# Kernel tuning notes

Measured on AMD Instinct MI355X. Metric: run time of the kernel, lower is better.

Reference implementation:

```python
import jax, jax.numpy as jnp
import numpy as np
from jax import lax


def _conv(x, w, b):
    y = lax.conv_general_dilated(x, w, window_strides=(1, 1), padding='SAME',
                                 dimension_numbers=('NCHW', 'OIHW', 'NCHW'))
    return y + b[None, :, None, None]


def _maxpool2(x):
    return lax.reduce_window(x, -jnp.inf, lax.max,
                             window_dimensions=(1, 1, 2, 2),
                             window_strides=(1, 1, 2, 2), padding='VALID')


def setup_inputs() -> dict:
    key = jax.random.key(0)
    ks = jax.random.split(key, 11)
    f32 = jnp.float32
    return {
        'x': jax.random.normal(ks[0], (512, 1, 112, 112), f32),
        'w_conv1': jax.random.normal(ks[1], (8, 1, 3, 3), f32) * 0.1,
        'b_conv1': jax.random.normal(ks[2], (8,), f32) * 0.1,
        'w_conv2': jax.random.normal(ks[3], (16, 8, 3, 3), f32) * 0.1,
        'b_conv2': jax.random.normal(ks[4], (16,), f32) * 0.1,
        'w_patch': jax.random.normal(ks[5], (4, 64), f32) * 0.1,
        'b_patch': jax.random.normal(ks[6], (4,), f32) * 0.1,
        'w_fc1': jax.random.normal(ks[7], (64, 784), f32) * 0.05,
        'b_fc1': jax.random.normal(ks[8], (64,), f32) * 0.05,
        'w_fc2': jax.random.normal(ks[9], (10, 64), f32) * 0.05,
        'b_fc2': jax.random.normal(ks[10], (10,), f32) * 0.05,
    }


def reference(x, w_conv1, b_conv1, w_conv2, b_conv2, w_patch, b_patch,
              w_fc1, b_fc1, w_fc2, b_fc2):
    B = x.shape[0]
    h = _maxpool2(jax.nn.relu(_conv(x, w_conv1, b_conv1)))        # [B,8,56,56]
    f = _maxpool2(jax.nn.relu(_conv(h, w_conv2, b_conv2)))        # [B,16,28,28]
    C, H, W = f.shape[1], f.shape[2], f.shape[3]
    # im2col: 2x2 non-overlapping spatial patches, flattened as (C,2,2) -> 64
    p = f.reshape(B, C, H // 2, 2, W // 2, 2)
    p = p.transpose(0, 2, 4, 1, 3, 5).reshape(B, (H // 2) * (W // 2), C * 4)  # [B,196,64]
    pf = jnp.einsum('bpk,ok->bpo', p, w_patch) + b_patch          # [B,196,4]
    pf = pf.reshape(B, -1)                                        # [B,784]
    h1 = jax.nn.relu(pf @ w_fc1.T + b_fc1)
    logits = h1 @ w_fc2.T + b_fc2
    return jax.nn.log_softmax(logits, axis=-1)
```

## Files before the change

### kernel.cpp

```cpp
#include <hip/hip_runtime.h>


#define HS 58
#define FSTR 33

typedef _Float16 half2_t __attribute__((ext_vector_type(2)));
typedef _Float16 f16x8 __attribute__((ext_vector_type(8)));
typedef float f32x4 __attribute__((ext_vector_type(4)));
typedef float f32x2 __attribute__((ext_vector_type(2)));

__device__ __forceinline__ unsigned pack_f16(float a, float b) {
  union { half2_t h; unsigned u; } z;
  z.h[0] = (_Float16)a;
  z.h[1] = (_Float16)b;
  return z.u;
}

__device__ __forceinline__ half2_t as_h2(unsigned u) {
  union { unsigned u; half2_t h; } z;
  z.u = u;
  return z.h;
}

__device__ __forceinline__ f16x8 as_f16x8(uint4 u) {
  union { uint4 u; f16x8 f; } z;
  z.u = u;
  return z.f;
}

__device__ __forceinline__ float fdot2_(half2_t a, half2_t b, float c) {
#if __has_builtin(__builtin_amdgcn_fdot2)
  return __builtin_amdgcn_fdot2(a, b, c, false);
#else
  return c + (float)a[0] * (float)b[0] + (float)a[1] * (float)b[1];
#endif
}

__global__ __launch_bounds__(1024, 8) void k_all(
    const float* __restrict__ x, const float* __restrict__ w1,
    const float* __restrict__ b1, const float* __restrict__ w2,
    const float* __restrict__ b2, const float* __restrict__ wp,
    const float* __restrict__ bp, const float* __restrict__ w_fc1,
    const float* __restrict__ b_fc1, const float* __restrict__ w_fc2,
    const float* __restrict__ b_fc2, float* __restrict__ out) {
  __shared__ __align__(16) unsigned hsu[HS * HS * 4];
  __shared__ __align__(16) unsigned bwl[768];
  __shared__ __align__(16) unsigned wps[128];
  __shared__ __align__(16) unsigned fsu[98 * FSTR];
  __shared__ __align__(16) float pfl[784];
  __shared__ float h1s[64];
  const int tid = threadIdx.x;
  const int b = blockIdx.x;
  const int l = tid & 63;
  const int wv = __builtin_amdgcn_readfirstlane(tid >> 6);
  const float* xb = x + (long)b * 12544;
  const float bpv = bp[tid & 3];

  if (tid < 228) {
    int i = tid, hr, hc;
    if (i < 58) { hr = 0; hc = i; }
    else if (i < 116) { hr = 57; hc = i - 58; }
    else if (i < 172) { hr = i - 115; hc = 0; }
    else { hr = i - 171; hc = 57; }
    *(uint4*)(hsu + (hr * HS + hc) * 4) = make_uint4(0u, 0u, 0u, 0u);
  }
  if (tid < 768) {
    int t = tid, oc = t / 48, rem = t - oc * 48;
    int tap = rem >> 2, w = rem & 3;
    unsigned v = 0u;
    if (tap < 9)
      v = pack_f16(w2[(oc * 8 + 2 * w) * 9 + tap],
                   w2[(oc * 8 + 2 * w + 1) * 9 + tap]);
    bwl[t] = v;
  }
  if (tid >= 768 && tid < 896) {
    int t = tid - 768;
    int i = t >> 2, ot = t & 3;
    int l0 = 2 * i, l1 = 2 * i + 1;
    wps[t] = pack_f16(wp[ot * 64 + (l0 & 15) * 4 + (l0 >> 4)],
                      wp[ot * 64 + (l1 & 15) * 4 + (l1 >> 4)]);
  }

  for (int task = tid; task < 3136; task += 1024) {
    int gr = task / 56, gc = task - gr * 56;
    float win[4][4];
    int iy0 = 2 * gr - 1, ix0 = 2 * gc - 1;
    if (gr >= 1 && gr <= 54 && gc >= 1 && gc <= 54) {
      const float* xp = xb + iy0 * 112 + ix0;
#pragma unroll
      for (int rr = 0; rr < 4; ++rr)
#pragma unroll
        for (int qq = 0; qq < 4; ++qq)
          win[rr][qq] = xp[rr * 112 + qq];
    } else {
#pragma unroll
      for (int rr = 0; rr < 4; ++rr) {
        int iy = iy0 + rr;
        bool yok = (unsigned)iy < 112u;
#pragma unroll
        for (int qq = 0; qq < 4; ++qq) {
          int ix = ix0 + qq;
          win[rr][qq] = (yok && (unsigned)ix < 112u) ? xb[iy * 112 + ix] : 0.f;
        }
      }
    }
    float hv[8];
#pragma unroll
    for (int ch = 0; ch < 8; ++ch) {
      f32x2 sA = {0.f, 0.f};
      f32x2 sB = {0.f, 0.f};
#pragma unroll
      for (int ty = 0; ty < 3; ++ty)
#pragma unroll
        for (int tx = 0; tx < 3; ++tx) {
          float wk = w1[ch * 9 + ty * 3 + tx];
          f32x2 wkk = {wk, wk};
          f32x2 xa = {win[ty][tx], win[ty][tx + 1]};
          f32x2 xb2 = {win[ty + 1][tx], win[ty + 1][tx + 1]};
          sA = __builtin_elementwise_fma(xa, wkk, sA);
          sB = __builtin_elementwise_fma(xb2, wkk, sB);
        }
      f32x2 sm = __builtin_elementwise_max(sA, sB);
      float m = fmaxf(sm.x, sm.y);
      hv[ch] = fmaxf(m + b1[ch], 0.f);
    }
    uint4 hw;
    hw.x = pack_f16(hv[0], hv[1]);
    hw.y = pack_f16(hv[2], hv[3]);
    hw.z = pack_f16(hv[4], hv[5]);
    hw.w = pack_f16(hv[6], hv[7]);
    *(uint4*)(hsu + ((gr + 1) * HS + gc + 1) * 4) = hw;
  }
  __syncthreads();

  {
    const int q = l >> 4;
    const int yoff = 2 * ((l >> 3) & 1) + ((l >> 1) & 1);
    const int xoff = 2 * ((l >> 2) & 1) + (l & 1);
    int poff[3];
#pragma unroll
    for (int kk = 0; kk < 3; ++kk) {
      int t = kk * 4 + q;
      int tt = t < 9 ? t : 8;
      int ty = tt / 3, tx = tt - ty * 3;
      poff[kk] = ((yoff + ty) * HS + xoff + tx) * 4;
    }
    uint4 bu0 = *(const uint4*)(bwl + ((l & 15) * 12 + 0 + q) * 4);
    uint4 bu1 = *(const uint4*)(bwl + ((l & 15) * 12 + 4 + q) * 4);
    uint4 bu2 = *(const uint4*)(bwl + ((l & 15) * 12 + 8 + q) * 4);
    const float b2v = b2[l & 15];
    _Float16* fsh = (_Float16*)fsu;

    for (int c = 0; c < 2; ++c) {
#pragma unroll 2
      for (int p_l = wv; p_l < 98; p_l += 16) {
        int p = c * 98 + p_l;
        int py = p / 14, px = p - py * 14;
        int pb = (4 * py * HS + 4 * px) * 4;
        uint4 a0u = *(const uint4*)(hsu + pb + poff[0]);
        uint4 a1u = *(const uint4*)(hsu + pb + poff[1]);
        uint4 a2u = *(const uint4*)(hsu + pb + poff[2]);
        f32x4 acc = {0.f, 0.f, 0.f, 0.f};
        acc = __builtin_amdgcn_mfma_f32_16x16x32_f16(as_f16x8(a0u), as_f16x8(bu0), acc, 0, 0, 0);
        acc = __builtin_amdgcn_mfma_f32_16x16x32_f16(as_f16x8(a1u), as_f16x8(bu1), acc, 0, 0, 0);
        acc = __builtin_amdgcn_mfma_f32_16x16x32_f16(as_f16x8(a2u), as_f16x8(bu2), acc, 0, 0, 0);
        float mx = fmaxf(fmaxf(acc[0], acc[1]), fmaxf(acc[2], acc[3]));
        float fv = fmaxf(mx + b2v, 0.f);
        fsh[p_l * (2 * FSTR) + l] = (_Float16)fv;
      }
      __syncthreads();
      if (tid < 392) {
        int row = tid >> 2, ot = tid & 3;
        const unsigned* fr = fsu + row * FSTR;
        float acc = 0.f;
#pragma unroll
        for (int i = 0; i < 32; ++i)
          acc = fdot2_(as_h2(fr[i]), as_h2(wps[i * 4 + ot]), acc);
        pfl[(c * 98 + row) * 4 + ot] = acc + bpv;
      }
      __syncthreads();
    }
  }

  {
    int j = tid >> 4, q16 = tid & 15;
    const float* wrow = w_fc1 + j * 784;
    float acc = 0.f;
    for (int lp = q16; lp < 196; lp += 16) {
      float4 w4 = *(const float4*)(wrow + lp * 4);
      float4 p4 = *(const float4*)(pfl + lp * 4);
      acc += w4.x * p4.x + w4.y * p4.y + w4.z * p4.z + w4.w * p4.w;
    }
    acc += __shfl_down(acc, 8, 16);
    acc += __shfl_down(acc, 4, 16);
    acc += __shfl_down(acc, 2, 16);
    acc += __shfl_down(acc, 1, 16);
    if (q16 == 0) h1s[j] = fmaxf(acc + b_fc1[j], 0.f);
  }
  __syncthreads();

  if (wv == 0) {
    float h = h1s[l];
    float lg[10];
#pragma unroll
    for (int o = 0; o < 10; ++o) {
      float t = h * w_fc2[o * 64 + l];
#pragma unroll
      for (int off = 32; off; off >>= 1) t += __shfl_xor(t, off);
      lg[o] = t + b_fc2[o];
    }
    float mx = lg[0];
#pragma unroll
    for (int o = 1; o < 10; ++o) mx = fmaxf(mx, lg[o]);
    float se = 0.f;
#pragma unroll
    for (int o = 0; o < 10; ++o) se += __expf(lg[o] - mx);
    float ls = mx + __logf(se);
#pragma unroll
    for (int o = 0; o < 10; ++o)
      if (l == o) out[b * 10 + o] = lg[o] - ls;
  }
}

extern "C" void kernel_launch(void* const* d_in, const int* in_sizes, int n_in,
                              void* d_out, int out_size, void* d_ws, size_t ws_size,
                              hipStream_t stream) {
  const float* x = (const float*)d_in[0];
  const float* w1 = (const float*)d_in[1];
  const float* b1 = (const float*)d_in[2];
  const float* w2 = (const float*)d_in[3];
  const float* b2 = (const float*)d_in[4];
  const float* wp = (const float*)d_in[5];
  const float* bp = (const float*)d_in[6];
  const float* wf1 = (const float*)d_in[7];
  const float* bf1 = (const float*)d_in[8];
  const float* wf2 = (const float*)d_in[9];
  const float* bf2 = (const float*)d_in[10];
  (void)d_ws; (void)ws_size;

  k_all<<<dim3(512), 1024, 0, stream>>>(x, w1, b1, w2, b2, wp, bp, wf1, bf1,
                                        wf2, bf2, (float*)d_out);
}
```

Before: 116.4 us.

## Compute patch projection per-wave with MFMA and drop block-wide barriers

Each wave now owns a contiguous range of 12-13 patches and writes its conv2 outputs into a private LDS scratch region. It then runs the 64->4 patch projection itself with two MFMA instructions instead of a separate 392-thread fdot2 phase. This removes four block-wide __syncthreads and the serialized dot-product stage, replacing them with a per-wave lgkmcnt wait. The conv1 window rows are also loaded as 4-wide vectors. Correctness depends on the wave-local scratch layout, and the MFMA only fills a few of its output rows and columns, so some compute is wasted.

```diff
diff --git a/kernel.cpp b/kernel.cpp
--- a/kernel.cpp
+++ b/kernel.cpp
@@ -2,12 +2,14 @@
 
 
 #define HS 58
-#define FSTR 33
+#define FS 72
+#define FSW 36
 
 typedef _Float16 half2_t __attribute__((ext_vector_type(2)));
 typedef _Float16 f16x8 __attribute__((ext_vector_type(8)));
 typedef float f32x4 __attribute__((ext_vector_type(4)));
 typedef float f32x2 __attribute__((ext_vector_type(2)));
+typedef float f32x4u __attribute__((ext_vector_type(4), aligned(4)));
 
 __device__ __forceinline__ unsigned pack_f16(float a, float b) {
   union { half2_t h; unsigned u; } z;
@@ -16,24 +18,10 @@
   return z.u;
 }
 
-__device__ __forceinline__ half2_t as_h2(unsigned u) {
-  union { unsigned u; half2_t h; } z;
-  z.u = u;
-  return z.h;
-}
-
 __device__ __forceinline__ f16x8 as_f16x8(uint4 u) {
   union { uint4 u; f16x8 f; } z;
   z.u = u;
   return z.f;
-}
-
-__device__ __forceinline__ float fdot2_(half2_t a, half2_t b, float c) {
-#if __has_builtin(__builtin_amdgcn_fdot2)
-  return __builtin_amdgcn_fdot2(a, b, c, false);
-#else
-  return c + (float)a[0] * (float)b[0] + (float)a[1] * (float)b[1];
-#endif
 }
 
 __global__ __launch_bounds__(1024, 8) void k_all(
@@ -45,8 +33,7 @@
     const float* __restrict__ b_fc2, float* __restrict__ out) {
   __shared__ __align__(16) unsigned hsu[HS * HS * 4];
   __shared__ __align__(16) unsigned bwl[768];
-  __shared__ __align__(16) unsigned wps[128];
-  __shared__ __align__(16) unsigned fsu[98 * FSTR];
+  __shared__ __align__(16) unsigned fsu[122 * FSW];
   __shared__ __align__(16) float pfl[784];
   __shared__ float h1s[64];
   const int tid = threadIdx.x;
@@ -54,7 +41,6 @@
   const int l = tid & 63;
   const int wv = __builtin_amdgcn_readfirstlane(tid >> 6);
   const float* xb = x + (long)b * 12544;
-  const float bpv = bp[tid & 3];
 
   if (tid < 228) {
     int i = tid, hr, hc;
@@ -73,13 +59,6 @@
                    w2[(oc * 8 + 2 * w + 1) * 9 + tap]);
     bwl[t] = v;
   }
-  if (tid >= 768 && tid < 896) {
-    int t = tid - 768;
-    int i = t >> 2, ot = t & 3;
-    int l0 = 2 * i, l1 = 2 * i + 1;
-    wps[t] = pack_f16(wp[ot * 64 + (l0 & 15) * 4 + (l0 >> 4)],
-                      wp[ot * 64 + (l1 & 15) * 4 + (l1 >> 4)]);
-  }
 
   for (int task = tid; task < 3136; task += 1024) {
     int gr = task / 56, gc = task - gr * 56;
@@ -88,10 +67,10 @@
     if (gr >= 1 && gr <= 54 && gc >= 1 && gc <= 54) {
       const float* xp = xb + iy0 * 112 + ix0;
 #pragma unroll
-      for (int rr = 0; rr < 4; ++rr)
-#pragma unroll
-        for (int qq = 0; qq < 4; ++qq)
-          win[rr][qq] = xp[rr * 112 + qq];
+      for (int rr = 0; rr < 4; ++rr) {
+        f32x4u v = *(const f32x4u*)(xp + rr * 112);
+        win[rr][0] = v.x; win[rr][1] = v.y; win[rr][2] = v.z; win[rr][3] = v.w;
+      }
     } else {
 #pragma unroll
       for (int rr = 0; rr < 4; ++rr) {
@@ -135,6 +114,7 @@
 
   {
     const int q = l >> 4;
+    const int oc = l & 15;
     const int yoff = 2 * ((l >> 3) & 1) + ((l >> 1) & 1);
     const int xoff = 2 * ((l >> 2) & 1) + (l & 1);
     int poff[3];
@@ -145,16 +125,44 @@
       int ty = tt / 3, tx = tt - ty * 3;
       poff[kk] = ((yoff + ty) * HS + xoff + tx) * 4;
     }
-    uint4 bu0 = *(const uint4*)(bwl + ((l & 15) * 12 + 0 + q) * 4);
-    uint4 bu1 = *(const uint4*)(bwl + ((l & 15) * 12 + 4 + q) * 4);
-    uint4 bu2 = *(const uint4*)(bwl + ((l & 15) * 12 + 8 + q) * 4);
-    const float b2v = b2[l & 15];
+    uint4 bu0 = *(const uint4*)(bwl + (oc * 12 + 0 + q) * 4);
+    uint4 bu1 = *(const uint4*)(bwl + (oc * 12 + 4 + q) * 4);
+    uint4 bu2 = *(const uint4*)(bwl + (oc * 12 + 8 + q) * 4);
+    const float b2v = b2[oc];
+
+    f16x8 wpf0 = {}, wpf1 = {};
+    float bpj = 0.f;
+    if (oc < 4) {
+      const float* wr = wp + oc * 64 + q * 8;
+      float4 wa = *(const float4*)(wr);
+      float4 wb = *(const float4*)(wr + 4);
+      float4 wc = *(const float4*)(wr + 32);
+      float4 wd = *(const float4*)(wr + 36);
+      union { unsigned u[4]; f16x8 v; } u0, u1;
+      u0.u[0] = pack_f16(wa.x, wa.y);
+      u0.u[1] = pack_f16(wa.z, wa.w);
+      u0.u[2] = pack_f16(wb.x, wb.y);
+      u0.u[3] = pack_f16(wb.z, wb.w);
+      u1.u[0] = pack_f16(wc.x, wc.y);
+      u1.u[1] = pack_f16(wc.z, wc.w);
+      u1.u[2] = pack_f16(wd.x, wd.y);
+      u1.u[3] = pack_f16(wd.z, wd.w);
+      wpf0 = u0.v;
+      wpf1 = u1.v;
+      bpj = bp[oc];
+    }
+
     _Float16* fsh = (_Float16*)fsu;
-
-    for (int c = 0; c < 2; ++c) {
-#pragma unroll 2
-      for (int p_l = wv; p_l < 98; p_l += 16) {
-        int p = c * 98 + p_l;
+    const int NP = (wv < 4) ? 13 : 12;
+    const int G0 = (wv < 4) ? 13 * wv : 12 * wv + 4;
+    const int RW = 7 * wv;
+    const int npA = (NP + 1) >> 1;
+
+    for (int hlf = 0; hlf < 2; ++hlf) {
+      const int np = hlf ? NP - npA : npA;
+      const int g0 = hlf ? G0 + npA : G0;
+      for (int i = 0; i < np; ++i) {
+        int p = g0 + i;
         int py = p / 14, px = p - py * 14;
         int pb = (4 * py * HS + 4 * px) * 4;
         uint4 a0u = *(const uint4*)(hsu + pb + poff[0]);
@@ -166,21 +174,27 @@
         acc = __builtin_amdgcn_mfma_f32_16x16x32_f16(as_f16x8(a2u), as_f16x8(bu2), acc, 0, 0, 0);
         float mx = fmaxf(fmaxf(acc[0], acc[1]), fmaxf(acc[2], acc[3]));
         float fv = fmaxf(mx + b2v, 0.f);
-        fsh[p_l * (2 * FSTR) + l] = (_Float16)fv;
-      }
-      __syncthreads();
-      if (tid < 392) {
-        int row = tid >> 2, ot = tid & 3;
-        const unsigned* fr = fsu + row * FSTR;
-        float acc = 0.f;
-#pragma unroll
-        for (int i = 0; i < 32; ++i)
-          acc = fdot2_(as_h2(fr[i]), as_h2(wps[i * 4 + ot]), acc);
-        pfl[(c * 98 + row) * 4 + ot] = acc + bpv;
-      }
-      __syncthreads();
-    }
-  }
+        fsh[(RW + i) * FS + oc * 4 + q] = (_Float16)fv;
+      }
+      asm volatile("s_waitcnt lgkmcnt(0)" ::: "memory");
+      __builtin_amdgcn_sched_barrier(0);
+      const unsigned* ar = fsu + (RW + oc) * FSW + q * 4;
+      uint4 pa0 = *(const uint4*)(ar);
+      uint4 pa1 = *(const uint4*)(ar + 16);
+      f32x4 pc = {0.f, 0.f, 0.f, 0.f};
+      pc = __builtin_amdgcn_mfma_f32_16x16x32_f16(as_f16x8(pa0), wpf0, pc, 0, 0, 0);
+      pc = __builtin_amdgcn_mfma_f32_16x16x32_f16(as_f16x8(pa1), wpf1, pc, 0, 0, 0);
+      if (oc < 4) {
+#pragma unroll
+        for (int i2 = 0; i2 < 4; ++i2) {
+          int prow = q * 4 + i2;
+          if (prow < np) pfl[(g0 + prow) * 4 + oc] = pc[i2] + bpj;
+        }
+      }
+      asm volatile("" ::: "memory");
+    }
+  }
+  __syncthreads();
 
   {
     int j = tid >> 4, q16 = tid & 15;
```

New measurement: 116.1 us. No clear change (-0.3%).
